# Optimization experiments

Hardware: AMD Instinct MI355X
Metric: run time of the kernel (lower is better)

Reference implementation:

```python
import jax, jax.numpy as jnp
import numpy as np

TEMP = 1.0
EULER_GAMMA = 0.5772156649015329
BIG = 1.0e9


def setup_inputs() -> dict:
    key = jax.random.key(0)
    k = jax.random.split(key, 8)
    B, N, D, H = 32, 1024, 1024, 512  # batch, seq, d_model, hidden_size//2
    queries = jax.random.normal(k[0], (B, N, D), jnp.float32)
    queries_mask = jnp.ones((B, N), dtype=bool)
    W1 = jax.random.normal(k[1], (D, H), jnp.float32) * 0.02
    b1 = jnp.zeros((H,), jnp.float32)
    W2 = jax.random.normal(k[2], (H, 1), jnp.float32) * 0.02
    b2 = jnp.zeros((1,), jnp.float32)
    uniform_noise = jax.random.uniform(k[3], (B, N, 1), jnp.float32, 0.0, 1e-5)
    gumbel_noise = jax.random.gumbel(k[4], (B, N, 1), jnp.float32)
    return {"queries": queries, "queries_mask": queries_mask, "W1": W1, "b1": b1,
            "W2": W2, "b2": b2, "uniform_noise": uniform_noise,
            "gumbel_noise": gumbel_noise, "action_refinement": 1}


def reference(queries, queries_mask, W1, b1, W2, b2, uniform_noise, gumbel_noise, action_refinement):
    B, N, D = queries.shape
    # block0: Dense(H, relu) -> Dense(1); then softplus clamp + log + tiny uniform noise
    h = jax.nn.relu(jnp.einsum('bnd,dh->bnh', queries, W1) + b1)
    acts = jnp.einsum('bnh,ho->bno', h, W2) + b2                      # [B,N,1]
    acts = jnp.log(jnp.maximum(jax.nn.softplus(acts), 1e-5)) + uniform_noise
    acts = jnp.repeat(acts, action_refinement, axis=0)                # [BR,N,1]
    vmask = jnp.repeat(queries_mask[:, None, :].astype(jnp.float32), action_refinement, axis=0)  # [BR,1,N]
    n_valid = jnp.sum(vmask, axis=-1)                                 # [BR,1]
    mask_n1 = jnp.transpose(vmask, (0, 2, 1))                         # [BR,N,1]
    sqz_mask = mask_n1[..., 0]                                        # [BR,N]
    masked_acts = jnp.where(mask_n1 > 0, acts, -1e6)                  # [BR,N,1]
    perturb = masked_acts + gumbel_noise                              # [BR,N,1]
    # deterministic NeuralSort
    s = (jnp.exp(perturb) * mask_n1)[..., 0]                          # [BR,N]
    A = jnp.abs(s[:, :, None] - s[:, None, :])                        # [BR,N,N]
    Bmat = jnp.sum(A, axis=-1, keepdims=True)                         # A @ (1 1^T): row sums broadcast
    scaling = (N + 1 - 2 * (jnp.arange(N) + 1)).astype(jnp.float32)   # [N]
    C = s[:, :, None] * scaling[None, None, :]                        # [BR,N,N]
    P_hat = jnp.transpose(C - Bmat, (0, 2, 1)) - (1.0 - vmask) * BIG  # [BR,N,N]
    # greedy argmax permutation extraction (find_permu), vectorized over batch
    BR = P_hat.shape[0]
    def step(flag, row):                                              # row: [BR,N]
        tmp = row - flag * BIG
        idx = jnp.argmax(tmp, axis=-1)
        flag = jnp.maximum(flag, jax.nn.one_hot(idx, N, dtype=flag.dtype))
        return flag, idx
    _, idxs = jax.lax.scan(step, jnp.zeros((BR, N), jnp.float32), jnp.transpose(P_hat, (1, 0, 2)))
    chosen = jnp.transpose(idxs).astype(jnp.int32)                    # [BR,N]
    chosen = jnp.concatenate([jnp.zeros((BR, 1), jnp.int32), chosen[:, :-1]], axis=-1)
    id_permu = jnp.arange(N, dtype=jnp.int32)[None, :]
    permu = jnp.where(sqz_mask > 0, chosen, id_permu)                 # [BR,N]
    sample_permu = jax.nn.one_hot(permu, N, axis=-1, dtype=jnp.float32)
    # Plackett-Luce log-likelihood of sampled permutation
    exp_actis = jnp.exp(jnp.take_along_axis(masked_acts[..., 0], permu, axis=-1))
    rev_cumsum = jnp.cumsum(exp_actis[:, ::-1], axis=-1)[:, ::-1]
    eps = 1e-20
    log_nom = (jnp.log(exp_actis + eps) - jnp.log(rev_cumsum + eps)) * sqz_mask
    log_nom = jnp.sum(log_nom, axis=-1, keepdims=True)                # [BR,1]
    log_norm = jnp.zeros_like(log_nom)
    # KL term
    sqz_acts = acts[..., 0]
    kl1 = n_valid * (np.log(TEMP) - 1.0 + EULER_GAMMA * (1.0 / TEMP - 1.0))
    s1 = (1.0 / TEMP) * jnp.sum(sqz_acts * sqz_mask, axis=-1).reshape(-1, 1)
    s2 = jnp.sum(jnp.exp(-1.0 / TEMP * jnp.maximum(sqz_acts * sqz_mask, -20.0 * TEMP)), axis=-1).reshape(-1, 1) - (jnp.float32(N) - n_valid)
    kl = kl1 + s1 + s2 * jnp.exp(jax.lax.lgamma(jnp.float32(1.0 + 1.0 / TEMP)))
    return sample_permu, masked_acts[..., 0], kl, log_nom, log_norm
```

## Files before the change

kernel.cpp:

```cpp
#include <hip/hip_runtime.h>
#include <math.h>

#define BB 32
#define NN 1024
#define DD 1024
#define HH 512

#define OUT0_OFF 0
#define OUT1_OFF (BB * NN * NN)
#define OUT2_OFF (OUT1_OFF + BB * NN)
#define OUT3_OFF (OUT2_OFF + BB)
#define OUT4_OFF (OUT3_OFF + BB)

#define WS_ACTS 0
#define WS_W1T  131072
#define WS_RANK 1179648

typedef __attribute__((ext_vector_type(8))) short short8;
typedef __attribute__((ext_vector_type(4))) float floatx4;

__device__ inline unsigned int f2bf(float x) {
    unsigned int u = __builtin_bit_cast(unsigned int, x);
    return (u + 0x7FFFu + ((u >> 16) & 1u)) >> 16;
}

__device__ inline void gload_lds16(const void* g, void* l) {
    __builtin_amdgcn_global_load_lds(
        (const __attribute__((address_space(1))) unsigned int*)g,
        (__attribute__((address_space(3))) unsigned int*)l, 16, 0, 0);
}

__global__ __launch_bounds__(1024) void w1t_kernel(const float* __restrict__ W1,
                                                   unsigned short* __restrict__ W1T)
{
    __shared__ float T[32][33];
    const int tx = threadIdx.x, ty = threadIdx.y;
    const int d0 = blockIdx.x * 32, h0 = blockIdx.y * 32;
    T[ty][tx] = W1[(d0 + ty) * HH + h0 + tx];
    __syncthreads();
    W1T[(size_t)(h0 + ty) * DD + d0 + tx] = (unsigned short)f2bf(T[tx][ty]);
}

#define MT 64
#define SB() __builtin_amdgcn_sched_barrier(0)

__global__ __launch_bounds__(512, 4) void gemm_acts_kernel(
    const float* __restrict__ q, const unsigned short* __restrict__ W1T,
    const float* __restrict__ b1, const float* __restrict__ W2,
    const float* __restrict__ b2, const float* __restrict__ unoise,
    float* __restrict__ acts_ws, float* __restrict__ out1)
{
    __shared__ short As[2][MT * 64];
    __shared__ short Bs[2][HH * 32];

    const int tid  = threadIdx.x;
    const int w    = tid >> 6;
    const int lane = tid & 63;
    const int c    = lane & 15;
    const int qd   = lane >> 4;
    const int m0   = blockIdx.x * MT;

    floatx4 acc[4][4];
    #pragma unroll
    for (int tn = 0; tn < 4; ++tn)
        #pragma unroll
        for (int tm = 0; tm < 4; ++tm)
            acc[tn][tm] = (floatx4){0.f, 0.f, 0.f, 0.f};

    int boff[4];
    #pragma unroll
    for (int j = 0; j < 4; ++j) {
        int n  = (w * 4 + j) * 16 + (lane >> 2);
        int c0 = (lane & 3) * 16;
        int s  = (n >> 1) & 3;
        boff[j] = n * 2048 + (c0 ^ (s << 4));
    }
    const char* w1tb = (const char*)W1T;

    const int arow = tid >> 3;
    const int agrp = tid & 7;
    const float* aptrA = q + (size_t)(m0 + arow) * DD + ((agrp ^ (arow & 7)) * 8);
    const int adst = arow * 128 + agrp * 16;

    int aoffA[4], aoffB[4], boffr[4];
    #pragma unroll
    for (int tm = 0; tm < 4; ++tm) {
        int r = tm * 16 + c;
        aoffA[tm] = r * 128 + 16 * ((qd)     ^ (r & 7));
        aoffB[tm] = r * 128 + 16 * ((4 + qd) ^ (r & 7));
    }
    #pragma unroll
    for (int tn = 0; tn < 4; ++tn) {
        int n = w * 64 + tn * 16 + c;
        boffr[tn] = n * 64 + ((qd * 16) ^ (((n >> 1) & 3) << 4));
    }

    float4 a0, a1;

    {
        float4 v0 = *(const float4*)(aptrA + 0);
        float4 v1 = *(const float4*)(aptrA + 4);
        uint4 pk;
        pk.x = f2bf(v0.x) | (f2bf(v0.y) << 16);
        pk.y = f2bf(v0.z) | (f2bf(v0.w) << 16);
        pk.z = f2bf(v1.x) | (f2bf(v1.y) << 16);
        pk.w = f2bf(v1.z) | (f2bf(v1.w) << 16);
        *(uint4*)((char*)(&As[0][0]) + adst) = pk;
    }
    SB();
    #pragma unroll
    for (int j = 0; j < 4; ++j)
        gload_lds16(w1tb + boff[j], (char*)(&Bs[0][0]) + (w * 4 + j) * 1024);
    SB();
    a0 = *(const float4*)(aptrA + 64);
    a1 = *(const float4*)(aptrA + 64 + 4);
    SB();
    #pragma unroll
    for (int j = 0; j < 4; ++j)
        gload_lds16(w1tb + (boff[j] + 64), (char*)(&Bs[1][0]) + (w * 4 + j) * 1024);
    SB();

    #pragma unroll 1
    for (int s = 0; s < 16; ++s) {
        const int p = s & 1;
        const char* asP = (const char*)(&As[p][0]);
        char*       asN = (char*)(&As[p ^ 1][0]);

        asm volatile("s_waitcnt lgkmcnt(0)" ::: "memory");
        __builtin_amdgcn_s_barrier();
        asm volatile("s_waitcnt vmcnt(6)" ::: "memory");

        {
            short8 af[4];
            #pragma unroll
            for (int tm = 0; tm < 4; ++tm)
                af[tm] = *(const short8*)(asP + aoffA[tm]);
            __builtin_amdgcn_s_setprio(1);
            #pragma unroll
            for (int tn = 0; tn < 4; ++tn) {
                short8 bf = *(const short8*)((const char*)(&Bs[0][0]) + boffr[tn]);
                #pragma unroll
                for (int tm = 0; tm < 4; ++tm)
                    acc[tn][tm] = __builtin_amdgcn_mfma_f32_16x16x32_bf16(
                        af[tm], bf, acc[tn][tm], 0, 0, 0);
            }
            __builtin_amdgcn_s_setprio(0);
        }
        SB();
        if (s < 15) {
            #pragma unroll
            for (int j = 0; j < 4; ++j)
                gload_lds16(w1tb + (boff[j] + (2 * s + 2) * 64),
                            (char*)(&Bs[0][0]) + (w * 4 + j) * 1024);
            SB();
            asm volatile("s_waitcnt vmcnt(4)" ::: "memory");
        } else {
            asm volatile("s_waitcnt vmcnt(0)" ::: "memory");
        }

        {
            short8 af[4];
            #pragma unroll
            for (int tm = 0; tm < 4; ++tm)
                af[tm] = *(const short8*)(asP + aoffB[tm]);
            if (s < 15) {
                uint4 pk;
                pk.x = f2bf(a0.x) | (f2bf(a0.y) << 16);
                pk.y = f2bf(a0.z) | (f2bf(a0.w) << 16);
                pk.z = f2bf(a1.x) | (f2bf(a1.y) << 16);
                pk.w = f2bf(a1.z) | (f2bf(a1.w) << 16);
                *(uint4*)(asN + adst) = pk;
                SB();
                const int ka = (s < 14) ? s + 2 : 15;
                a0 = *(const float4*)(aptrA + ka * 64);
                a1 = *(const float4*)(aptrA + ka * 64 + 4);
                SB();
            }
            __builtin_amdgcn_s_setprio(1);
            #pragma unroll
            for (int tn = 0; tn < 4; ++tn) {
                short8 bf = *(const short8*)((const char*)(&Bs[1][0]) + boffr[tn]);
                #pragma unroll
                for (int tm = 0; tm < 4; ++tm)
                    acc[tn][tm] = __builtin_amdgcn_mfma_f32_16x16x32_bf16(
                        af[tm], bf, acc[tn][tm], 0, 0, 0);
            }
            __builtin_amdgcn_s_setprio(0);
        }
        SB();
        if (s < 15) {
            #pragma unroll
            for (int j = 0; j < 4; ++j)
                gload_lds16(w1tb + (boff[j] + (2 * s + 3) * 64),
                            (char*)(&Bs[1][0]) + (w * 4 + j) * 1024);
            SB();
        }
    }

    float (*red)[8] = (float (*)[8])(&As[0][0]);
    float b1v[4], w2v[4];
    #pragma unroll
    for (int tn = 0; tn < 4; ++tn) {
        int col = w * 64 + tn * 16 + c;
        b1v[tn] = b1[col];
        w2v[tn] = W2[col];
    }
    __syncthreads();
    #pragma unroll
    for (int tm = 0; tm < 4; ++tm) {
        #pragma unroll
        for (int r = 0; r < 4; ++r) {
            float p = 0.f;
            #pragma unroll
            for (int tn = 0; tn < 4; ++tn) {
                float v = acc[tn][tm][r] + b1v[tn];
                p = fmaf(fmaxf(v, 0.f), w2v[tn], p);
            }
            p += __shfl_xor(p, 1);
            p += __shfl_xor(p, 2);
            p += __shfl_xor(p, 4);
            p += __shfl_xor(p, 8);
            if (c == 0) red[tm * 16 + qd * 4 + r][w] = p;
        }
    }
    __syncthreads();
    if (tid < MT) {
        float raw = red[tid][0] + red[tid][1] + red[tid][2] + red[tid][3] +
                    red[tid][4] + red[tid][5] + red[tid][6] + red[tid][7] + b2[0];
        float sp = fmaxf(raw, 0.f) + log1pf(expf(-fabsf(raw)));
        int row = m0 + tid;
        float av = logf(fmaxf(sp, 1e-5f)) + unoise[row];
        acts_ws[row] = av;
        out1[row]    = av;
    }
}

__global__ __launch_bounds__(256) void zero_kernel(float4* __restrict__ p, int n4)
{
    int idx = blockIdx.x * blockDim.x + threadIdx.x;
    int stride = gridDim.x * blockDim.x;
    float4 z = make_float4(0.f, 0.f, 0.f, 0.f);
    for (int i = idx; i < n4; i += stride) p[i] = z;
}

__global__ __launch_bounds__(256) void rank_kernel(
    const float* __restrict__ acts_ws, const float* __restrict__ gumbel,
    int* __restrict__ rank)
{
    __shared__ float P[NN];
    const int b = blockIdx.x >> 2;
    const int chunk = blockIdx.x & 3;
    const int tid = threadIdx.x;
    #pragma unroll
    for (int r = 0; r < 4; ++r) {
        int j = r * 256 + tid;
        P[j] = acts_ws[b * NN + j] + gumbel[b * NN + j];
    }
    __syncthreads();
    const int i = chunk * 256 + tid;
    const float pert = P[i];
    int cnt = 0;
    const float4* P4 = (const float4*)P;
    for (int j4 = 0; j4 < NN / 4; ++j4) {
        float4 pv = P4[j4];
        int j = j4 * 4;
        cnt += (pv.x > pert) || (pv.x == pert && j + 0 < i);
        cnt += (pv.y > pert) || (pv.y == pert && j + 1 < i);
        cnt += (pv.z > pert) || (pv.z == pert && j + 2 < i);
        cnt += (pv.w > pert) || (pv.w == pert && j + 3 < i);
    }
    rank[b * NN + i] = cnt;
}

__global__ __launch_bounds__(1024) void permu_stats_kernel(
    const float* __restrict__ acts_ws, const int* __restrict__ rank,
    float* __restrict__ out0, float* __restrict__ out2,
    float* __restrict__ out3, float* __restrict__ out4)
{
    __shared__ float A[NN];
    __shared__ int   IDX[NN];
    __shared__ float WT[16];
    __shared__ float WSUF[17];
    __shared__ float P0[16], P1[16], P2[16];

    const int b = blockIdx.x;
    const int i = threadIdx.x;
    const int lane = i & 63;
    const int w = i >> 6;

    float a = acts_ws[b * NN + i];
    A[i] = a;
    IDX[rank[b * NN + i]] = i;
    __syncthreads();

    int perm = (i == 0) ? 0 : IDX[i - 1];
    out0[((size_t)b * NN + i) * NN + perm] = 1.0f;

    float e = expf(A[perm]);
    float s = e;
    #pragma unroll
    for (int off = 1; off < 64; off <<= 1) {
        float v = __shfl_down(s, off);
        if (lane + off < 64) s += v;
    }
    if (lane == 0) WT[w] = s;
    __syncthreads();
    if (w == 0) {
        float t = (lane < 16) ? WT[lane] : 0.f;
        #pragma unroll
        for (int off = 1; off < 16; off <<= 1) {
            float v = __shfl_down(t, off);
            if (lane + off < 16) t += v;
        }
        if (lane < 16) WSUF[lane] = t;
        if (lane == 0) WSUF[16] = 0.f;
    }
    __syncthreads();

    float S = s + WSUF[w + 1];
    float term = logf(e + 1e-20f) - logf(S + 1e-20f);

    float r0 = term, r1 = a, r2 = expf(-fmaxf(a, -20.f));
    #pragma unroll
    for (int off = 1; off < 64; off <<= 1) {
        r0 += __shfl_xor(r0, off);
        r1 += __shfl_xor(r1, off);
        r2 += __shfl_xor(r2, off);
    }
    if (lane == 0) { P0[w] = r0; P1[w] = r1; P2[w] = r2; }
    __syncthreads();
    if (i == 0) {
        float t0 = 0.f, t1 = 0.f, t2 = 0.f;
        #pragma unroll
        for (int k = 0; k < 16; ++k) { t0 += P0[k]; t1 += P1[k]; t2 += P2[k]; }
        out3[b] = t0;
        out2[b] = -(float)NN + t1 + t2;
        out4[b] = 0.f;
    }
}

extern "C" void kernel_launch(void* const* d_in, const int* in_sizes, int n_in,
                              void* d_out, int out_size, void* d_ws, size_t ws_size,
                              hipStream_t stream)
{
    const float* q      = (const float*)d_in[0];
    const float* W1     = (const float*)d_in[2];
    const float* b1     = (const float*)d_in[3];
    const float* W2     = (const float*)d_in[4];
    const float* b2     = (const float*)d_in[5];
    const float* unoise = (const float*)d_in[6];
    const float* gumbel = (const float*)d_in[7];

    float* out  = (float*)d_out;
    char*  ws   = (char*)d_ws;
    float*          acts = (float*)(ws + WS_ACTS);
    unsigned short* W1T  = (unsigned short*)(ws + WS_W1T);
    int*            rank = (int*)(ws + WS_RANK);

    w1t_kernel<<<dim3(32, 16), dim3(32, 32), 0, stream>>>(W1, W1T);
    gemm_acts_kernel<<<(BB * NN) / MT, 512, 0, stream>>>(q, W1T, b1, W2, b2,
                                                         unoise, acts,
                                                         out + OUT1_OFF);
    zero_kernel<<<8192, 256, 0, stream>>>((float4*)(out + OUT0_OFF),
                                          (BB * NN * NN) / 4);
    rank_kernel<<<BB * 4, 256, 0, stream>>>(acts, gumbel, rank);
    permu_stats_kernel<<<BB, 1024, 0, stream>>>(acts, rank,
                                                out + OUT0_OFF, out + OUT2_OFF,
                                                out + OUT3_OFF, out + OUT4_OFF);
}
```

Before: 320.4 us.

## Load W1T fragments directly from global into registers instead of staging in LDS

```diff
diff --git a/kernel.cpp b/kernel.cpp
--- a/kernel.cpp
+++ b/kernel.cpp
@@ -24,12 +24,6 @@
     return (u + 0x7FFFu + ((u >> 16) & 1u)) >> 16;
 }
 
-__device__ inline void gload_lds16(const void* g, void* l) {
-    __builtin_amdgcn_global_load_lds(
-        (const __attribute__((address_space(1))) unsigned int*)g,
-        (__attribute__((address_space(3))) unsigned int*)l, 16, 0, 0);
-}
-
 __global__ __launch_bounds__(1024) void w1t_kernel(const float* __restrict__ W1,
                                                    unsigned short* __restrict__ W1T)
 {
@@ -42,7 +36,6 @@
 }
 
 #define MT 64
-#define SB() __builtin_amdgcn_sched_barrier(0)
 
 __global__ __launch_bounds__(512, 4) void gemm_acts_kernel(
     const float* __restrict__ q, const unsigned short* __restrict__ W1T,
@@ -51,7 +44,7 @@
     float* __restrict__ acts_ws, float* __restrict__ out1)
 {
     __shared__ short As[2][MT * 64];
-    __shared__ short Bs[2][HH * 32];
+    __shared__ float red[MT][8];
 
     const int tid  = threadIdx.x;
     const int w    = tid >> 6;
@@ -67,32 +60,23 @@
         for (int tm = 0; tm < 4; ++tm)
             acc[tn][tm] = (floatx4){0.f, 0.f, 0.f, 0.f};
 
-    int boff[4];
-    #pragma unroll
-    for (int j = 0; j < 4; ++j) {
-        int n  = (w * 4 + j) * 16 + (lane >> 2);
-        int c0 = (lane & 3) * 16;
-        int s  = (n >> 1) & 3;
-        boff[j] = n * 2048 + (c0 ^ (s << 4));
-    }
-    const char* w1tb = (const char*)W1T;
+    const short8* w1ts = (const short8*)W1T;
+    int bunit[4];
+    #pragma unroll
+    for (int tn = 0; tn < 4; ++tn)
+        bunit[tn] = (w * 64 + tn * 16 + c) * 128 + qd;
 
     const int arow = tid >> 3;
     const int agrp = tid & 7;
     const float* aptrA = q + (size_t)(m0 + arow) * DD + ((agrp ^ (arow & 7)) * 8);
     const int adst = arow * 128 + agrp * 16;
 
-    int aoffA[4], aoffB[4], boffr[4];
+    int aoffA[4], aoffB[4];
     #pragma unroll
     for (int tm = 0; tm < 4; ++tm) {
         int r = tm * 16 + c;
         aoffA[tm] = r * 128 + 16 * ((qd)     ^ (r & 7));
         aoffB[tm] = r * 128 + 16 * ((4 + qd) ^ (r & 7));
-    }
-    #pragma unroll
-    for (int tn = 0; tn < 4; ++tn) {
-        int n = w * 64 + tn * 16 + c;
-        boffr[tn] = n * 64 + ((qd * 16) ^ (((n >> 1) & 3) << 4));
     }
 
     float4 a0, a1;
@@ -106,98 +90,60 @@
         pk.z = f2bf(v1.x) | (f2bf(v1.y) << 16);
         pk.w = f2bf(v1.z) | (f2bf(v1.w) << 16);
         *(uint4*)((char*)(&As[0][0]) + adst) = pk;
-    }
-    SB();
-    #pragma unroll
-    for (int j = 0; j < 4; ++j)
-        gload_lds16(w1tb + boff[j], (char*)(&Bs[0][0]) + (w * 4 + j) * 1024);
-    SB();
-    a0 = *(const float4*)(aptrA + 64);
-    a1 = *(const float4*)(aptrA + 64 + 4);
-    SB();
-    #pragma unroll
-    for (int j = 0; j < 4; ++j)
-        gload_lds16(w1tb + (boff[j] + 64), (char*)(&Bs[1][0]) + (w * 4 + j) * 1024);
-    SB();
+        a0 = *(const float4*)(aptrA + 64);
+        a1 = *(const float4*)(aptrA + 64 + 4);
+    }
 
     #pragma unroll 1
     for (int s = 0; s < 16; ++s) {
         const int p = s & 1;
         const char* asP = (const char*)(&As[p][0]);
         char*       asN = (char*)(&As[p ^ 1][0]);
-
-        asm volatile("s_waitcnt lgkmcnt(0)" ::: "memory");
-        __builtin_amdgcn_s_barrier();
-        asm volatile("s_waitcnt vmcnt(6)" ::: "memory");
+        __syncthreads();
 
         {
-            short8 af[4];
-            #pragma unroll
-            for (int tm = 0; tm < 4; ++tm)
-                af[tm] = *(const short8*)(asP + aoffA[tm]);
-            __builtin_amdgcn_s_setprio(1);
-            #pragma unroll
-            for (int tn = 0; tn < 4; ++tn) {
-                short8 bf = *(const short8*)((const char*)(&Bs[0][0]) + boffr[tn]);
+            short8 bf[4];
+            #pragma unroll
+            for (int tn = 0; tn < 4; ++tn)
+                bf[tn] = w1ts[bunit[tn] + 8 * s];
+            #pragma unroll
+            for (int tm = 0; tm < 4; ++tm) {
+                short8 af = *(const short8*)(asP + aoffA[tm]);
                 #pragma unroll
-                for (int tm = 0; tm < 4; ++tm)
+                for (int tn = 0; tn < 4; ++tn)
                     acc[tn][tm] = __builtin_amdgcn_mfma_f32_16x16x32_bf16(
-                        af[tm], bf, acc[tn][tm], 0, 0, 0);
+                        af, bf[tn], acc[tn][tm], 0, 0, 0);
             }
-            __builtin_amdgcn_s_setprio(0);
-        }
-        SB();
+        }
+
         if (s < 15) {
-            #pragma unroll
-            for (int j = 0; j < 4; ++j)
-                gload_lds16(w1tb + (boff[j] + (2 * s + 2) * 64),
-                            (char*)(&Bs[0][0]) + (w * 4 + j) * 1024);
-            SB();
-            asm volatile("s_waitcnt vmcnt(4)" ::: "memory");
-        } else {
-            asm volatile("s_waitcnt vmcnt(0)" ::: "memory");
+            uint4 pk;
+            pk.x = f2bf(a0.x) | (f2bf(a0.y) << 16);
+            pk.y = f2bf(a0.z) | (f2bf(a0.w) << 16);
+            pk.z = f2bf(a1.x) | (f2bf(a1.y) << 16);
+            pk.w = f2bf(a1.z) | (f2bf(a1.w) << 16);
+            *(uint4*)(asN + adst) = pk;
+            const int ka = (s < 14) ? s + 2 : 15;
+            a0 = *(const float4*)(aptrA + ka * 64);
+            a1 = *(const float4*)(aptrA + ka * 64 + 4);
         }
 
         {
-            short8 af[4];
-            #pragma unroll
-            for (int tm = 0; tm < 4; ++tm)
-                af[tm] = *(const short8*)(asP + aoffB[tm]);
-            if (s < 15) {
-                uint4 pk;
-                pk.x = f2bf(a0.x) | (f2bf(a0.y) << 16);
-                pk.y = f2bf(a0.z) | (f2bf(a0.w) << 16);
-                pk.z = f2bf(a1.x) | (f2bf(a1.y) << 16);
-                pk.w = f2bf(a1.z) | (f2bf(a1.w) << 16);
-                *(uint4*)(asN + adst) = pk;
-                SB();
-                const int ka = (s < 14) ? s + 2 : 15;
-                a0 = *(const float4*)(aptrA + ka * 64);
-                a1 = *(const float4*)(aptrA + ka * 64 + 4);
-                SB();
+            short8 bf[4];
+            #pragma unroll
+            for (int tn = 0; tn < 4; ++tn)
+                bf[tn] = w1ts[bunit[tn] + 8 * s + 4];
+            #pragma unroll
+            for (int tm = 0; tm < 4; ++tm) {
+                short8 af = *(const short8*)(asP + aoffB[tm]);
+                #pragma unroll
+                for (int tn = 0; tn < 4; ++tn)
+                    acc[tn][tm] = __builtin_amdgcn_mfma_f32_16x16x32_bf16(
+                        af, bf[tn], acc[tn][tm], 0, 0, 0);
             }
-            __builtin_amdgcn_s_setprio(1);
-            #pragma unroll
-            for (int tn = 0; tn < 4; ++tn) {
-                short8 bf = *(const short8*)((const char*)(&Bs[1][0]) + boffr[tn]);
-                #pragma unroll
-                for (int tm = 0; tm < 4; ++tm)
-                    acc[tn][tm] = __builtin_amdgcn_mfma_f32_16x16x32_bf16(
-                        af[tm], bf, acc[tn][tm], 0, 0, 0);
-            }
-            __builtin_amdgcn_s_setprio(0);
-        }
-        SB();
-        if (s < 15) {
-            #pragma unroll
-            for (int j = 0; j < 4; ++j)
-                gload_lds16(w1tb + (boff[j] + (2 * s + 3) * 64),
-                            (char*)(&Bs[1][0]) + (w * 4 + j) * 1024);
-            SB();
-        }
-    }
-
-    float (*red)[8] = (float (*)[8])(&As[0][0]);
+        }
+    }
+
     float b1v[4], w2v[4];
     #pragma unroll
     for (int tn = 0; tn < 4; ++tn) {
@@ -205,7 +151,6 @@
         b1v[tn] = b1[col];
         w2v[tn] = W2[col];
     }
-    __syncthreads();
     #pragma unroll
     for (int tm = 0; tm < 4; ++tm) {
         #pragma unroll
```

New measurement: 334.5 us. 1.04x slower.
